# Kernel optimization log

Measured on AMD Instinct MI355X. Metric: run time of the kernel, lower is better.

Reference implementation:

```python
import jax, jax.numpy as jnp
import numpy as np

B, S, HID, NH = 2, 2048, 1024, 16
HD = HID // NH

def setup_inputs() -> dict:
    key = jax.random.key(0)
    ks = jax.random.split(key, 9)
    s = 1.0 / np.sqrt(HID)
    return {
        "hidden_state": jax.random.normal(ks[0], (B, S, HID), jnp.float32),
        "Wq": jax.random.normal(ks[1], (HID, HID), jnp.float32) * s,
        "bq": jax.random.normal(ks[2], (HID,), jnp.float32) * 0.02,
        "Wk": jax.random.normal(ks[3], (HID, HID), jnp.float32) * s,
        "bk": jax.random.normal(ks[4], (HID,), jnp.float32) * 0.02,
        "Wv": jax.random.normal(ks[5], (HID, HID), jnp.float32) * s,
        "bv": jax.random.normal(ks[6], (HID,), jnp.float32) * 0.02,
        "Wo": jax.random.normal(ks[7], (HID, HID), jnp.float32) * s,
        "bo": jax.random.normal(ks[8], (HID,), jnp.float32) * 0.02,
    }

def _split_heads(x):
    # [B,S,HID] -> [B,NH,S,HD]
    b, s, _ = x.shape
    return x.reshape(b, s, NH, HD).transpose(0, 2, 1, 3)

def reference(hidden_state, Wq, bq, Wk, bk, Wv, bv, Wo, bo):
    # torch nn.Linear: y = x @ W.T + b
    q = _split_heads(hidden_state @ Wq.T + bq)
    k = _split_heads(hidden_state @ Wk.T + bk)
    v = _split_heads(hidden_state @ Wv.T + bv)
    scale = 1.0 / jnp.sqrt(jnp.asarray(HD, hidden_state.dtype))
    scores = jnp.einsum("bhqd,bhkd->bhqk", q, k) * scale
    probs = jax.nn.softmax(scores, axis=-1)
    out = jnp.einsum("bhqk,bhkd->bhqd", probs, v)  # [B,NH,S,HD]
    out = out.transpose(0, 2, 1, 3).reshape(hidden_state.shape[0], -1, NH * HD)
    return out @ Wo.T + bo
```

## Files before the change

### kernel.cpp

```cpp
#include <hip/hip_runtime.h>


#define S_LEN 2048
#define HID   1024
#define NHEAD 16
#define HDIM  64
#define M_TOT 4096
#define LOG2E 1.4426950408889634f

typedef __attribute__((ext_vector_type(8))) short bf16x8;
typedef __attribute__((ext_vector_type(4))) float f32x4;

static __device__ __forceinline__ float b2f(short s) {
  union { unsigned int u; float f; } v;
  v.u = ((unsigned int)(unsigned short)s) << 16;
  return v.f;
}
static __device__ __forceinline__ short f2b(float f) {
  union { unsigned int u; float f; } v; v.f = f;
  unsigned int r = (v.u + 0x7FFFu + ((v.u >> 16) & 1u)) >> 16;
  return (short)(unsigned short)r;
}
static __device__ __forceinline__ short f2b_fast(float f) {
  union { unsigned int u; float f; } v; v.f = f;
  return (short)(unsigned short)((v.u + 0x8000u) >> 16);
}
static __device__ __forceinline__ float fexp2(float x) { return exp2f(x); }

#define GLD_LDS16(g, l)                                                        \
  __builtin_amdgcn_global_load_lds(                                            \
      (const __attribute__((address_space(1))) void*)(g),                      \
      (__attribute__((address_space(3))) void*)(l), 16, 0, 0)

__global__ __launch_bounds__(256) void convert_all_kernel(
    const float* s0, const float* s1, const float* s2, const float* s3,
    const float* s4, const float* s5, const float* s6, const float* s7,
    const float* s8,
    short* d0, short* d1, short* d2, short* d3, short* d4,
    short* d5, short* d6, short* d7, short* d8)
{
  const float* src; short* dst; int n;
  switch (blockIdx.y) {
    case 0: src = s0; dst = d0; n = M_TOT * HID; break;
    case 1: src = s1; dst = d1; n = HID * HID; break;
    case 2: src = s2; dst = d2; n = HID; break;
    case 3: src = s3; dst = d3; n = HID * HID; break;
    case 4: src = s4; dst = d4; n = HID; break;
    case 5: src = s5; dst = d5; n = HID * HID; break;
    case 6: src = s6; dst = d6; n = HID; break;
    case 7: src = s7; dst = d7; n = HID * HID; break;
    default: src = s8; dst = d8; n = HID; break;
  }
  const int stride = gridDim.x * 256 * 4;
  int i = (blockIdx.x * 256 + threadIdx.x) * 4;
  for (; i < n; i += stride) {
    float4 v = *(const float4*)(src + i);
    ushort4 o;
    o.x = (unsigned short)f2b(v.x); o.y = (unsigned short)f2b(v.y);
    o.z = (unsigned short)f2b(v.z); o.w = (unsigned short)f2b(v.w);
    *(ushort4*)(dst + i) = o;
  }
}

__global__ __launch_bounds__(256) void gemm_qkv_kernel(
    const short* __restrict__ X,
    const short* __restrict__ Wq, const short* __restrict__ Wk, const short* __restrict__ Wv,
    const short* __restrict__ bq, const short* __restrict__ bk, const short* __restrict__ bv,
    short* __restrict__ Q, short* __restrict__ K, short* __restrict__ V)
{
  __shared__ short Alds[8704];
  __shared__ short Wlds[64 * 64];
  const int ntile = blockIdx.y;
  const int which = ntile >> 4;
  const int n0    = (ntile & 15) * 64;
  const int bm    = blockIdx.x * 128;
  const short* W    = (which == 0) ? Wq : (which == 1) ? Wk : Wv;
  const short* bias = (which == 0) ? bq : (which == 1) ? bk : bv;

  const int t    = threadIdx.x;
  const int lane = t & 63;
  const int w    = t >> 6;
  const int quad = lane >> 4, l15 = lane & 15;

  f32x4 acc[2][4];
#pragma unroll
  for (int i = 0; i < 2; ++i)
#pragma unroll
    for (int j = 0; j < 4; ++j) acc[i][j] = (f32x4){0.f, 0.f, 0.f, 0.f};

  {
    const int srow = t >> 3;
    const int cg   = (t & 7) ^ (srow & 7);
    const short* Ag = X + (size_t)(bm + srow) * HID + cg * 8;
    const short* Wg = W + (size_t)(n0 + srow) * HID + cg * 8;

    for (int k0 = 0; k0 < HID; k0 += 64) {
      __syncthreads();
#pragma unroll
      for (int i = 0; i < 4; ++i)
        GLD_LDS16(Ag + (size_t)i * 32 * HID + k0, Alds + i * 2048 + t * 8);
#pragma unroll
      for (int i = 0; i < 2; ++i)
        GLD_LDS16(Wg + (size_t)i * 32 * HID + k0, Wlds + i * 2048 + t * 8);
      __syncthreads();

      bf16x8 af[2][2], bfr[4][2];
#pragma unroll
      for (int mt = 0; mt < 2; ++mt)
#pragma unroll
        for (int ks = 0; ks < 2; ++ks)
          af[mt][ks] = *(const bf16x8*)(Alds + (w * 32 + mt * 16 + l15) * 64 +
                                        (((ks * 4 + quad) ^ (l15 & 7)) * 8));
#pragma unroll
      for (int nt = 0; nt < 4; ++nt)
#pragma unroll
        for (int ks = 0; ks < 2; ++ks)
          bfr[nt][ks] = *(const bf16x8*)(Wlds + (nt * 16 + l15) * 64 +
                                         (((ks * 4 + quad) ^ (l15 & 7)) * 8));
#pragma unroll
      for (int mt = 0; mt < 2; ++mt)
#pragma unroll
        for (int nt = 0; nt < 4; ++nt) {
          acc[mt][nt] = __builtin_amdgcn_mfma_f32_16x16x32_bf16(af[mt][0], bfr[nt][0], acc[mt][nt], 0, 0, 0);
          acc[mt][nt] = __builtin_amdgcn_mfma_f32_16x16x32_bf16(af[mt][1], bfr[nt][1], acc[mt][nt], 0, 0, 0);
        }
    }
  }

  if (which != 2) {
    short* Out = (which == 0) ? Q : K;
    const float scl = (which == 0) ? 0.125f * LOG2E : 1.0f;
#pragma unroll
    for (int nt = 0; nt < 4; ++nt) {
      const int n = n0 + nt * 16 + l15;
      const float bvv = b2f(bias[n]);
#pragma unroll
      for (int mt = 0; mt < 2; ++mt)
#pragma unroll
        for (int r = 0; r < 4; ++r) {
          const int m = bm + w * 32 + mt * 16 + quad * 4 + r;
          Out[(size_t)m * HID + n] = f2b((acc[mt][nt][r] + bvv) * scl);
        }
    }
  } else {
    __syncthreads();
#pragma unroll
    for (int nt = 0; nt < 4; ++nt) {
      const int n = nt * 16 + l15;
      const float bvv = b2f(bias[n0 + n]);
#pragma unroll
      for (int mt = 0; mt < 2; ++mt) {
        const int m = w * 32 + mt * 16 + quad * 4;
#pragma unroll
        for (int r = 0; r < 4; r += 2) {
          union { unsigned int u; short s2[2]; } pk;
          pk.s2[0] = f2b(acc[mt][nt][r] + bvv);
          pk.s2[1] = f2b(acc[mt][nt][r + 1] + bvv);
          *(unsigned int*)(Alds + n * 136 + m + r) = pk.u;
        }
      }
    }
    __syncthreads();
    const int nr   = t >> 2;
    const int mseg = (t & 3) * 32;
    const int bb = bm >> 11, s0 = bm & 2047;
    short* dst = V + ((size_t)(bb * 1024 + n0 + nr)) * 2048 + s0 + mseg;
#pragma unroll
    for (int k = 0; k < 4; ++k)
      *(bf16x8*)(dst + k * 8) = *(const bf16x8*)(Alds + nr * 136 + mseg + k * 8);
  }
}

__global__ __launch_bounds__(256) void gemm_o_kernel(
    const short* __restrict__ A, const short* __restrict__ W,
    const short* __restrict__ bias, float* __restrict__ out)
{
  __shared__ short Alds[128 * 64];
  __shared__ short Wlds[64 * 64];
  const int n0 = blockIdx.y * 64;
  const int bm = blockIdx.x * 128;

  const int t    = threadIdx.x;
  const int lane = t & 63;
  const int w    = t >> 6;
  const int quad = lane >> 4, l15 = lane & 15;

  f32x4 acc[2][4];
#pragma unroll
  for (int i = 0; i < 2; ++i)
#pragma unroll
    for (int j = 0; j < 4; ++j) acc[i][j] = (f32x4){0.f, 0.f, 0.f, 0.f};

  const int srow = t >> 3;
  const int cg   = (t & 7) ^ (srow & 7);
  const short* Ag = A + (size_t)(bm + srow) * HID + cg * 8;
  const short* Wg = W + (size_t)(n0 + srow) * HID + cg * 8;

  for (int k0 = 0; k0 < HID; k0 += 64) {
    __syncthreads();
#pragma unroll
    for (int i = 0; i < 4; ++i)
      GLD_LDS16(Ag + (size_t)i * 32 * HID + k0, Alds + i * 2048 + t * 8);
#pragma unroll
    for (int i = 0; i < 2; ++i)
      GLD_LDS16(Wg + (size_t)i * 32 * HID + k0, Wlds + i * 2048 + t * 8);
    __syncthreads();

    bf16x8 af[2][2], bfr[4][2];
#pragma unroll
    for (int mt = 0; mt < 2; ++mt)
#pragma unroll
      for (int ks = 0; ks < 2; ++ks)
        af[mt][ks] = *(const bf16x8*)(Alds + (w * 32 + mt * 16 + l15) * 64 +
                                      (((ks * 4 + quad) ^ (l15 & 7)) * 8));
#pragma unroll
    for (int nt = 0; nt < 4; ++nt)
#pragma unroll
      for (int ks = 0; ks < 2; ++ks)
        bfr[nt][ks] = *(const bf16x8*)(Wlds + (nt * 16 + l15) * 64 +
                                       (((ks * 4 + quad) ^ (l15 & 7)) * 8));
#pragma unroll
    for (int mt = 0; mt < 2; ++mt)
#pragma unroll
      for (int nt = 0; nt < 4; ++nt) {
        acc[mt][nt] = __builtin_amdgcn_mfma_f32_16x16x32_bf16(af[mt][0], bfr[nt][0], acc[mt][nt], 0, 0, 0);
        acc[mt][nt] = __builtin_amdgcn_mfma_f32_16x16x32_bf16(af[mt][1], bfr[nt][1], acc[mt][nt], 0, 0, 0);
      }
  }

#pragma unroll
  for (int nt = 0; nt < 4; ++nt) {
    const int n = n0 + nt * 16 + l15;
    const float bvv = b2f(bias[n]);
#pragma unroll
    for (int mt = 0; mt < 2; ++mt)
#pragma unroll
      for (int r = 0; r < 4; ++r) {
        const int m = bm + w * 32 + mt * 16 + quad * 4 + r;
        out[(size_t)m * HID + n] = acc[mt][nt][r] + bvv;
      }
  }
}

__global__ __launch_bounds__(256) void flash_attn_kernel(
    const short* __restrict__ Q, const short* __restrict__ K,
    const short* __restrict__ V, short* __restrict__ O)
{
  __shared__ short Kl0[64 * 64], Kl1[64 * 64];
  __shared__ short Vl0[64 * 64], Vl1[64 * 64];
  __shared__ short Pl[4 * 32 * 64];

  const int t    = threadIdx.x;
  const int lane = t & 63, w = t >> 6;
  const int quad = lane >> 4, l15 = lane & 15;
  const int qtile = blockIdx.x;
  const int bh    = blockIdx.y;
  const int b = bh >> 4, h = bh & 15;
  const int hoff = h * HDIM;

  bf16x8 qf[2][2];
#pragma unroll
  for (int mt = 0; mt < 2; ++mt) {
    const int qrow = b * S_LEN + qtile * 128 + w * 32 + mt * 16 + l15;
#pragma unroll
    for (int ks = 0; ks < 2; ++ks)
      qf[mt][ks] = *(const bf16x8*)(Q + (size_t)qrow * HID + hoff + ks * 32 + quad * 8);
  }

  f32x4 o[2][4], ol[2];
#pragma unroll
  for (int mt = 0; mt < 2; ++mt) {
#pragma unroll
    for (int nt = 0; nt < 4; ++nt) o[mt][nt] = (f32x4){0.f, 0.f, 0.f, 0.f};
    ol[mt] = (f32x4){0.f, 0.f, 0.f, 0.f};
  }

  bf16x8 vones;
#pragma unroll
  for (int j = 0; j < 8; ++j) vones[j] = (short)0x3F80;

  short* myP = Pl + w * (32 * 64);
  const int srow = t >> 3;
  const int cg   = (t & 7) ^ (srow & 7);
  const short* Kg = K + (size_t)(b * S_LEN) * HID + hoff + cg * 8;
  const short* Vg = V + (size_t)(bh * HDIM) * S_LEN + cg * 8;

  auto stage = [&](short* dK, short* dV, int kv0) {
    GLD_LDS16(Kg + (size_t)(kv0 + srow) * HID,      dK + t * 8);
    GLD_LDS16(Kg + (size_t)(kv0 + 32 + srow) * HID, dK + 2048 + t * 8);
    GLD_LDS16(Vg + (size_t)srow * S_LEN + kv0,        dV + t * 8);
    GLD_LDS16(Vg + (size_t)(32 + srow) * S_LEN + kv0, dV + 2048 + t * 8);
  };

  auto step = [&](int it, const short* Kc, const short* Vc, short* Kn, short* Vn) {
    __syncthreads();
    if (it < 31) stage(Kn, Vn, (it + 1) * 64);

    bf16x8 kf[4][2];
#pragma unroll
    for (int kt = 0; kt < 4; ++kt)
#pragma unroll
      for (int ks = 0; ks < 2; ++ks)
        kf[kt][ks] = *(const bf16x8*)(Kc + (kt * 16 + l15) * 64 +
                                      (((ks * 4 + quad) ^ (l15 & 7)) * 8));

#pragma unroll
    for (int mt = 0; mt < 2; ++mt) {
      f32x4 s[4];
#pragma unroll
      for (int kt = 0; kt < 4; ++kt) {
        s[kt] = (f32x4){0.f, 0.f, 0.f, 0.f};
        s[kt] = __builtin_amdgcn_mfma_f32_16x16x32_bf16(qf[mt][0], kf[kt][0], s[kt], 0, 0, 0);
        s[kt] = __builtin_amdgcn_mfma_f32_16x16x32_bf16(qf[mt][1], kf[kt][1], s[kt], 0, 0, 0);
      }
      short* Pm = myP + mt * (16 * 64);
#pragma unroll
      for (int kt = 0; kt < 4; ++kt)
#pragma unroll
        for (int r = 0; r < 4; ++r)
          Pm[(quad * 4 + r) * 64 + (((kt * 2 + (l15 >> 3)) ^ quad) * 8) + (l15 & 7)] =
              f2b_fast(fexp2(s[kt][r]));
    }

    bf16x8 pa[2][2];
#pragma unroll
    for (int mt = 0; mt < 2; ++mt)
#pragma unroll
      for (int ks = 0; ks < 2; ++ks)
        pa[mt][ks] = *(const bf16x8*)(myP + (mt * 16 + l15) * 64 +
                                      (((ks * 4 + quad) ^ ((l15 >> 2) & 3)) * 8));

#pragma unroll
    for (int nt = 0; nt < 4; ++nt) {
#pragma unroll
      for (int ks = 0; ks < 2; ++ks) {
        bf16x8 vf = *(const bf16x8*)(Vc + (nt * 16 + l15) * 64 +
                                     (((ks * 4 + quad) ^ (l15 & 7)) * 8));
        o[0][nt] = __builtin_amdgcn_mfma_f32_16x16x32_bf16(pa[0][ks], vf, o[0][nt], 0, 0, 0);
        o[1][nt] = __builtin_amdgcn_mfma_f32_16x16x32_bf16(pa[1][ks], vf, o[1][nt], 0, 0, 0);
      }
    }
#pragma unroll
    for (int mt = 0; mt < 2; ++mt) {
      ol[mt] = __builtin_amdgcn_mfma_f32_16x16x32_bf16(pa[mt][0], vones, ol[mt], 0, 0, 0);
      ol[mt] = __builtin_amdgcn_mfma_f32_16x16x32_bf16(pa[mt][1], vones, ol[mt], 0, 0, 0);
    }
  };

  stage(Kl0, Vl0, 0);
#pragma unroll 1
  for (int it = 0; it < 32; it += 2) {
    step(it,     Kl0, Vl0, Kl1, Vl1);
    step(it + 1, Kl1, Vl1, Kl0, Vl0);
  }

#pragma unroll
  for (int mt = 0; mt < 2; ++mt) {
    const int orow = b * S_LEN + qtile * 128 + w * 32 + mt * 16 + quad * 4;
#pragma unroll
    for (int nt = 0; nt < 4; ++nt) {
      const int col = hoff + nt * 16 + l15;
#pragma unroll
      for (int r = 0; r < 4; ++r)
        O[(size_t)(orow + r) * HID + col] = f2b(o[mt][nt][r] / ol[mt][r]);
    }
  }
}

extern "C" void kernel_launch(void* const* d_in, const int* in_sizes, int n_in,
                              void* d_out, int out_size, void* d_ws, size_t ws_size,
                              hipStream_t stream) {
  short* WS  = (short*)d_ws;
  const size_t M1 = 1024 * 1024;
  short* Xc  = WS;
  short* Wqc = WS + 4 * M1;
  short* Wkc = WS + 5 * M1;
  short* Wvc = WS + 6 * M1;
  short* Woc = WS + 7 * M1;
  short* bqc = WS + 8 * M1;
  short* bkc = bqc + 1024;
  short* bvc = bkc + 1024;
  short* boc = bvc + 1024;
  short* Qb  = WS + 9 * M1;
  short* Kb  = WS + 13 * M1;
  short* Vt  = WS + 17 * M1;
  short* An  = WS + 21 * M1;

  convert_all_kernel<<<dim3(128, 9), 256, 0, stream>>>(
      (const float*)d_in[0], (const float*)d_in[1], (const float*)d_in[2],
      (const float*)d_in[3], (const float*)d_in[4], (const float*)d_in[5],
      (const float*)d_in[6], (const float*)d_in[7], (const float*)d_in[8],
      Xc, Wqc, bqc, Wkc, bkc, Wvc, bvc, Woc, boc);

  gemm_qkv_kernel<<<dim3(32, 48), 256, 0, stream>>>(
      Xc, Wqc, Wkc, Wvc, bqc, bkc, bvc, Qb, Kb, Vt);

  flash_attn_kernel<<<dim3(16, 32), 256, 0, stream>>>(Qb, Kb, Vt, An);

  gemm_o_kernel<<<dim3(32, 16), 256, 0, stream>>>(An, Woc, boc, (float*)d_out);
}
```

Measured before the change: 220.4 us.

## Keep softmax probabilities in registers via transposed S and 16x16x16 PV MFMA

Computes the score tile transposed (K as the A operand, Q as B) so each lane's accumulator holds the layout needed as the A operand of a 16x16x16 bf16 MFMA. The exponentiated probabilities then feed the PV product directly from registers, which removes the per-wave P shared-memory buffer and its write/read round trip. In exchange it issues twice as many smaller MFMAs for PV and the row-sum, and preloads V fragments as 4-element loads that hold more registers.

```diff
diff --git a/kernel.cpp b/kernel.cpp
--- a/kernel.cpp
+++ b/kernel.cpp
@@ -9,7 +9,14 @@
 #define LOG2E 1.4426950408889634f
 
 typedef __attribute__((ext_vector_type(8))) short bf16x8;
+typedef __attribute__((ext_vector_type(4))) short bf16x4;
 typedef __attribute__((ext_vector_type(4))) float f32x4;
+
+#if defined(__HIP_DEVICE_COMPILE__)
+#define MFMA16(a, b, c) __builtin_amdgcn_mfma_f32_16x16x16bf16_1k(a, b, c, 0, 0, 0)
+#else
+#define MFMA16(a, b, c) (c)
+#endif
 
 static __device__ __forceinline__ float b2f(short s) {
   union { unsigned int u; float f; } v;
@@ -248,7 +255,6 @@
 {
   __shared__ short Kl0[64 * 64], Kl1[64 * 64];
   __shared__ short Vl0[64 * 64], Vl1[64 * 64];
-  __shared__ short Pl[4 * 32 * 64];
 
   const int t    = threadIdx.x;
   const int lane = t & 63, w = t >> 6;
@@ -275,11 +281,10 @@
     ol[mt] = (f32x4){0.f, 0.f, 0.f, 0.f};
   }
 
-  bf16x8 vones;
-#pragma unroll
-  for (int j = 0; j < 8; ++j) vones[j] = (short)0x3F80;
-
-  short* myP = Pl + w * (32 * 64);
+  bf16x4 vones4;
+#pragma unroll
+  for (int j = 0; j < 4; ++j) vones4[j] = (short)0x3F80;
+
   const int srow = t >> 3;
   const int cg   = (t & 7) ^ (srow & 7);
   const short* Kg = K + (size_t)(b * S_LEN) * HID + hoff + cg * 8;
@@ -304,46 +309,39 @@
         kf[kt][ks] = *(const bf16x8*)(Kc + (kt * 16 + l15) * 64 +
                                       (((ks * 4 + quad) ^ (l15 & 7)) * 8));
 
+    bf16x4 vf[4][4];
+#pragma unroll
+    for (int kt = 0; kt < 4; ++kt)
+#pragma unroll
+      for (int nt = 0; nt < 4; ++nt)
+        vf[kt][nt] = *(const bf16x4*)(Vc + (nt * 16 + l15) * 64 +
+                                      (((2 * kt + (quad >> 1)) ^ (l15 & 7)) * 8) +
+                                      (quad & 1) * 4);
+
 #pragma unroll
     for (int mt = 0; mt < 2; ++mt) {
-      f32x4 s[4];
+      f32x4 st[4];
 #pragma unroll
       for (int kt = 0; kt < 4; ++kt) {
-        s[kt] = (f32x4){0.f, 0.f, 0.f, 0.f};
-        s[kt] = __builtin_amdgcn_mfma_f32_16x16x32_bf16(qf[mt][0], kf[kt][0], s[kt], 0, 0, 0);
-        s[kt] = __builtin_amdgcn_mfma_f32_16x16x32_bf16(qf[mt][1], kf[kt][1], s[kt], 0, 0, 0);
+        st[kt] = (f32x4){0.f, 0.f, 0.f, 0.f};
+        st[kt] = __builtin_amdgcn_mfma_f32_16x16x32_bf16(kf[kt][0], qf[mt][0], st[kt], 0, 0, 0);
+        st[kt] = __builtin_amdgcn_mfma_f32_16x16x32_bf16(kf[kt][1], qf[mt][1], st[kt], 0, 0, 0);
       }
-      short* Pm = myP + mt * (16 * 64);
+      bf16x4 p[4];
 #pragma unroll
       for (int kt = 0; kt < 4; ++kt)
 #pragma unroll
-        for (int r = 0; r < 4; ++r)
-          Pm[(quad * 4 + r) * 64 + (((kt * 2 + (l15 >> 3)) ^ quad) * 8) + (l15 & 7)] =
-              f2b_fast(fexp2(s[kt][r]));
-    }
-
-    bf16x8 pa[2][2];
-#pragma unroll
-    for (int mt = 0; mt < 2; ++mt)
-#pragma unroll
-      for (int ks = 0; ks < 2; ++ks)
-        pa[mt][ks] = *(const bf16x8*)(myP + (mt * 16 + l15) * 64 +
-                                      (((ks * 4 + quad) ^ ((l15 >> 2) & 3)) * 8));
-
-#pragma unroll
-    for (int nt = 0; nt < 4; ++nt) {
-#pragma unroll
-      for (int ks = 0; ks < 2; ++ks) {
-        bf16x8 vf = *(const bf16x8*)(Vc + (nt * 16 + l15) * 64 +
-                                     (((ks * 4 + quad) ^ (l15 & 7)) * 8));
-        o[0][nt] = __builtin_amdgcn_mfma_f32_16x16x32_bf16(pa[0][ks], vf, o[0][nt], 0, 0, 0);
-        o[1][nt] = __builtin_amdgcn_mfma_f32_16x16x32_bf16(pa[1][ks], vf, o[1][nt], 0, 0, 0);
-      }
-    }
-#pragma unroll
-    for (int mt = 0; mt < 2; ++mt) {
-      ol[mt] = __builtin_amdgcn_mfma_f32_16x16x32_bf16(pa[mt][0], vones, ol[mt], 0, 0, 0);
-      ol[mt] = __builtin_amdgcn_mfma_f32_16x16x32_bf16(pa[mt][1], vones, ol[mt], 0, 0, 0);
+        for (int j = 0; j < 4; ++j)
+          p[kt][j] = f2b_fast(fexp2(st[kt][j]));
+
+#pragma unroll
+      for (int nt = 0; nt < 4; ++nt)
+#pragma unroll
+        for (int kt = 0; kt < 4; ++kt)
+          o[mt][nt] = MFMA16(p[kt], vf[kt][nt], o[mt][nt]);
+#pragma unroll
+      for (int kt = 0; kt < 4; ++kt)
+        ol[mt] = MFMA16(p[kt], vones4, ol[mt]);
     }
   };
 
```

New measurement: 221.6 us. Within noise of the previous version (+0.6%).
